# Kernel optimization log

Measured on AMD Instinct MI355X. Metric: run time of the kernel, lower is better.

## Reference

```python
import jax, jax.numpy as jnp
import numpy as np
import math

EMBED_DIM = 2048
NUM_HEADS = 32
GROUPS = 4
HEAD_DIM = EMBED_DIM // NUM_HEADS  # 64
HPG = NUM_HEADS // GROUPS          # heads per group = 8


def setup_inputs() -> dict:
    key = jax.random.key(0)
    k_x, k_wq, k_bq, k_wkv, k_bkv = jax.random.split(key, 5)
    B, L = 4, 4096
    scale = 1.0 / math.sqrt(EMBED_DIM)
    return {
        "x": jax.random.normal(k_x, (B, L, EMBED_DIM), dtype=jnp.float32),
        "Wq": jax.random.normal(k_wq, (EMBED_DIM, EMBED_DIM), dtype=jnp.float32) * scale,
        "bq": jax.random.normal(k_bq, (EMBED_DIM,), dtype=jnp.float32) * 0.01,
        "Wkv": jax.random.normal(k_wkv, (EMBED_DIM, 2 * HEAD_DIM * GROUPS), dtype=jnp.float32) * scale,
        "bkv": jax.random.normal(k_bkv, (2 * HEAD_DIM * GROUPS,), dtype=jnp.float32) * 0.01,
    }


def reference(x, Wq, bq, Wkv, bkv):
    B, L, _ = x.shape
    # projections
    q = (x @ Wq + bq).reshape(B, L, GROUPS, HPG, HEAD_DIM)          # blghd
    kv = (x @ Wkv + bkv).reshape(B, L, GROUPS, 2, HEAD_DIM)
    k, v = kv[:, :, :, 0], kv[:, :, :, 1]                            # blgd
    # scores: q @ k^T with k of shape (..., 1, head_dim) -> (..., HPG, 1)
    scores = jnp.einsum("blghd,blgd->blgh", q, k)[..., None] / math.sqrt(HEAD_DIM)
    attn = jax.nn.softmax(scores, axis=-1)                           # size-1 axis -> ones
    # attn @ v: (..., HPG, 1) @ (..., 1, head_dim) -> (..., HPG, head_dim)
    out = attn * v[:, :, :, None, :]                                 # blghd
    return out.reshape(B, L, EMBED_DIM)
```

## Files before the change

kernel.cpp:

```cpp
#include <hip/hip_runtime.h>


#define EMBED 2048
#define SV 272

typedef _Float16 half8 __attribute__((ext_vector_type(8)));
typedef _Float16 half4v __attribute__((ext_vector_type(4)));
typedef float f32x4 __attribute__((ext_vector_type(4)));

#define GLOAD16(g, l)                                                      \
  __builtin_amdgcn_global_load_lds(                                        \
      (const __attribute__((address_space(1))) void*)(g),                  \
      (__attribute__((address_space(3))) void*)(l), 16, 0, 0)

__global__ __launch_bounds__(256) void prep_b(const float* __restrict__ Wkv,
                                              _Float16* __restrict__ Bt) {
  const int t = threadIdx.x;
  const int kb = blockIdx.x * 4;
  const int vcol = ((t >> 6) * 128) + 64 + (t & 63);
  float v[4];
#pragma unroll
  for (int i = 0; i < 4; ++i) v[i] = Wkv[(size_t)(kb + i) * 512 + vcol];
  half4v h;
#pragma unroll
  for (int i = 0; i < 4; ++i) h[i] = (_Float16)v[i];
  *(half4v*)&Bt[(size_t)t * EMBED + kb] = h;
}

__global__ __launch_bounds__(256) void gqa_main(
    const float* __restrict__ x, const _Float16* __restrict__ Bt,
    const float* __restrict__ bkv, float* __restrict__ out) {
  __shared__ __align__(16) char smem[4 * 8192 + 4 * 16384];
  char* const Ab = smem;
  char* const Bb = smem + 4 * 8192;
  float* const Vs = (float*)smem;

  const int tid = threadIdx.x;
  const int w = tid >> 6;
  const int lane = tid & 63;
  const int lm = lane & 15;
  const int lq = lane >> 4;
  const int row0 = blockIdx.x * 64;

  const int acol = ((lane & 7) ^ (lane >> 3)) << 4;
  const char* asrc0 = (const char*)x +
      (size_t)(row0 + w * 16 + (lane >> 3)) * (EMBED * 4) + acol;
  const char* asrc1 = asrc0 + (size_t)8 * EMBED * 4;
  const int adst0 = (w * 16) * 128;
  const int bcol = (((lane & 3) << 4) ^ (((lane >> 3) & 3) << 4));
  const char* bsrc0 = (const char*)Bt +
      (size_t)(w * 64 + (lane >> 2)) * (EMBED * 2) + bcol;
  const int bdst0 = (w * 64) * 64;

#define STAGE(b, s)                                                        \
  {                                                                        \
    const size_t sa_ = (size_t)(s) * 128;          \
    GLOAD16(asrc0 + sa_, Ab + (b) * 8192 + adst0);                         \
    GLOAD16(asrc1 + sa_, Ab + (b) * 8192 + adst0 + 1024);                  \
    const size_t sb_ = (size_t)(s) * 64;           \
    GLOAD16(bsrc0 + sb_, Bb + (b) * 16384 + bdst0);                        \
    GLOAD16(bsrc0 + sb_ + (size_t)16 * EMBED * 2,                          \
            Bb + (b) * 16384 + bdst0 + 1024);                              \
    GLOAD16(bsrc0 + sb_ + (size_t)32 * EMBED * 2,                          \
            Bb + (b) * 16384 + bdst0 + 2048);                              \
    GLOAD16(bsrc0 + sb_ + (size_t)48 * EMBED * 2,                          \
            Bb + (b) * 16384 + bdst0 + 3072);                              \
  }

  const int arswz = (lm & 7) << 4;
  const int brswz = ((lm >> 1) & 3) << 4;

#define COMPUTE(b)                                                         \
  {                                                                        \
    const char* Ar_ = Ab + (b) * 8192 + lm * 128;                          \
    const char* Br_ = Bb + (b) * 16384 + (w * 64 + lm) * 64 +              \
                      ((lq << 4) ^ brswz);                                 \
    half8 bf_[4];                                                          \
    _Pragma("unroll") for (int ni = 0; ni < 4; ++ni)                       \
        bf_[ni] = *(const half8*)(Br_ + ni * 1024);                        \
    _Pragma("unroll") for (int mi = 0; mi < 4; ++mi) {                     \
      f32x4 a0_ = *(const f32x4*)(Ar_ + mi * 2048 + ((lq << 5) ^ arswz));  \
      f32x4 a1_ = *(const f32x4*)(Ar_ + mi * 2048 + (((lq << 5) + 16) ^ arswz)); \
      half8 af_;                                                           \
      _Pragma("unroll") for (int j = 0; j < 4; ++j) af_[j] = (_Float16)a0_[j]; \
      _Pragma("unroll") for (int j = 0; j < 4; ++j) af_[4 + j] = (_Float16)a1_[j]; \
      _Pragma("unroll") for (int ni = 0; ni < 4; ++ni)                     \
          acc[mi][ni] = __builtin_amdgcn_mfma_f32_16x16x32_f16(            \
              af_, bf_[ni], acc[mi][ni], 0, 0, 0);                         \
    }                                                                      \
  }

  f32x4 acc[4][4] = {};

  STAGE(0, 0);
  STAGE(1, 1);
  STAGE(2, 2);

  for (int tt = 0; tt < 64; tt += 4) {
#define ITER(T, BC, BS)                                                    \
    asm volatile("s_waitcnt vmcnt(12)" ::: "memory");                      \
    __builtin_amdgcn_s_barrier();                                          \
    {                                                                      \
      const int ss_ = (T) + 3 < 64 ? (T) + 3 : 63;                         \
      STAGE(BS, ss_);                                                      \
    }                                                                      \
    COMPUTE(BC);
    ITER(tt + 0, 0, 3)
    ITER(tt + 1, 1, 0)
    ITER(tt + 2, 2, 1)
    ITER(tt + 3, 3, 2)
#undef ITER
  }

  asm volatile("s_waitcnt vmcnt(0)" ::: "memory");
  __syncthreads();

  float bias[4];
#pragma unroll
  for (int ni = 0; ni < 4; ++ni) bias[ni] = bkv[w * 128 + 64 + ni * 16 + lm];

#pragma unroll
  for (int c = 0; c < 8; ++c) {
    const int mi = c >> 1;
    if ((lq >> 1) == (c & 1)) {
#pragma unroll
      for (int ni = 0; ni < 4; ++ni) {
        const int n = w * 64 + ni * 16 + lm;
        f32x4 v = acc[mi][ni];
#pragma unroll
        for (int r = 0; r < 4; ++r)
          Vs[((lq & 1) * 4 + r) * SV + n] = v[r] + bias[ni];
      }
    }
    __syncthreads();
    f32x4* out4 = (f32x4*)(out + (size_t)(row0 + c * 8) * EMBED);
#pragma unroll 4
    for (int i = 0; i < 16; ++i) {
      const int f = i * 256 + tid;
      const int row = f >> 9;
      const int c4 = f & 511;
      const int grp = c4 >> 7;
      const int d4 = c4 & 15;
      out4[(size_t)row * 512 + c4] =
          *(const f32x4*)&Vs[row * SV + grp * 64 + d4 * 4];
    }
    __syncthreads();
  }
}

extern "C" void kernel_launch(void* const* d_in, const int* in_sizes, int n_in,
                              void* d_out, int out_size, void* d_ws, size_t ws_size,
                              hipStream_t stream) {
  const float* x = (const float*)d_in[0];
  const float* Wkv = (const float*)d_in[3];
  const float* bkv = (const float*)d_in[4];
  float* out = (float*)d_out;
  _Float16* Bt = (_Float16*)d_ws;

  prep_b<<<512, 256, 0, stream>>>(Wkv, Bt);
  gqa_main<<<256, 256, 0, stream>>>(x, Bt, bkv, out);
}
```

Measured before the change: 265.9 us.

## Double K-depth per pipeline stage and split fragment loads from MFMA

Each pipeline stage now covers twice the K range, using 3 LDS buffers of 48KB instead of 4 buffers of 24KB, with prefetch distance reduced from 3 to 2. Each iteration loads the first half's fragments before issuing the next stage's global loads, then alternates MFMA with loading the second half. The aim is more bytes in flight per wave and fewer barriers per K, so the kernel hides global-memory latency better. The cost is a larger LDS footprint (144KB) and a shallower pipeline.

```diff
diff --git a/kernel.cpp b/kernel.cpp
--- a/kernel.cpp
+++ b/kernel.cpp
@@ -30,9 +30,9 @@
 __global__ __launch_bounds__(256) void gqa_main(
     const float* __restrict__ x, const _Float16* __restrict__ Bt,
     const float* __restrict__ bkv, float* __restrict__ out) {
-  __shared__ __align__(16) char smem[4 * 8192 + 4 * 16384];
+  __shared__ __align__(16) char smem[3 * 16384 + 3 * 32768];
   char* const Ab = smem;
-  char* const Bb = smem + 4 * 8192;
+  char* const Bb = smem + 3 * 16384;
   float* const Vs = (float*)smem;
 
   const int tid = threadIdx.x;
@@ -43,74 +43,91 @@
   const int row0 = blockIdx.x * 64;
 
   const int acol = ((lane & 7) ^ (lane >> 3)) << 4;
-  const char* asrc0 = (const char*)x +
+  const char* asrc = (const char*)x +
       (size_t)(row0 + w * 16 + (lane >> 3)) * (EMBED * 4) + acol;
-  const char* asrc1 = asrc0 + (size_t)8 * EMBED * 4;
   const int adst0 = (w * 16) * 128;
-  const int bcol = (((lane & 3) << 4) ^ (((lane >> 3) & 3) << 4));
-  const char* bsrc0 = (const char*)Bt +
+  const int bcol = (((lane & 3) ^ ((lane >> 3) & 3)) << 4);
+  const char* bsrc = (const char*)Bt +
       (size_t)(w * 64 + (lane >> 2)) * (EMBED * 2) + bcol;
   const int bdst0 = (w * 64) * 64;
 
 #define STAGE(b, s)                                                        \
   {                                                                        \
-    const size_t sa_ = (size_t)(s) * 128;          \
-    GLOAD16(asrc0 + sa_, Ab + (b) * 8192 + adst0);                         \
-    GLOAD16(asrc1 + sa_, Ab + (b) * 8192 + adst0 + 1024);                  \
-    const size_t sb_ = (size_t)(s) * 64;           \
-    GLOAD16(bsrc0 + sb_, Bb + (b) * 16384 + bdst0);                        \
-    GLOAD16(bsrc0 + sb_ + (size_t)16 * EMBED * 2,                          \
-            Bb + (b) * 16384 + bdst0 + 1024);                              \
-    GLOAD16(bsrc0 + sb_ + (size_t)32 * EMBED * 2,                          \
-            Bb + (b) * 16384 + bdst0 + 2048);                              \
-    GLOAD16(bsrc0 + sb_ + (size_t)48 * EMBED * 2,                          \
-            Bb + (b) * 16384 + bdst0 + 3072);                              \
+    const char* as_ = asrc + (size_t)(s) * 256;                            \
+    char* ad_ = Ab + (b) * 16384 + adst0;                                  \
+    GLOAD16(as_, ad_);                                                     \
+    GLOAD16(as_ + (size_t)8 * EMBED * 4, ad_ + 1024);                      \
+    GLOAD16(as_ + 128, ad_ + 8192);                                        \
+    GLOAD16(as_ + (size_t)8 * EMBED * 4 + 128, ad_ + 8192 + 1024);         \
+    const char* bs_ = bsrc + (size_t)(s) * 128;                            \
+    char* bd_ = Bb + (b) * 32768 + bdst0;                                  \
+    GLOAD16(bs_, bd_);                                                     \
+    GLOAD16(bs_ + (size_t)16 * EMBED * 2, bd_ + 1024);                     \
+    GLOAD16(bs_ + (size_t)32 * EMBED * 2, bd_ + 2048);                     \
+    GLOAD16(bs_ + (size_t)48 * EMBED * 2, bd_ + 3072);                     \
+    GLOAD16(bs_ + 64, bd_ + 16384);                                        \
+    GLOAD16(bs_ + (size_t)16 * EMBED * 2 + 64, bd_ + 16384 + 1024);        \
+    GLOAD16(bs_ + (size_t)32 * EMBED * 2 + 64, bd_ + 16384 + 2048);        \
+    GLOAD16(bs_ + (size_t)48 * EMBED * 2 + 64, bd_ + 16384 + 3072);        \
   }
 
   const int arswz = (lm & 7) << 4;
   const int brswz = ((lm >> 1) & 3) << 4;
 
-#define COMPUTE(b)                                                         \
+#define LOADFRAG(b, roa, rob)                                              \
   {                                                                        \
-    const char* Ar_ = Ab + (b) * 8192 + lm * 128;                          \
-    const char* Br_ = Bb + (b) * 16384 + (w * 64 + lm) * 64 +              \
+    const char* Ar_ = Ab + (b) * 16384 + (roa) + lm * 128;                 \
+    const char* Br_ = Bb + (b) * 32768 + (rob) + (w * 64 + lm) * 64 +      \
                       ((lq << 4) ^ brswz);                                 \
-    half8 bf_[4];                                                          \
     _Pragma("unroll") for (int ni = 0; ni < 4; ++ni)                       \
-        bf_[ni] = *(const half8*)(Br_ + ni * 1024);                        \
+        bfr_[ni] = *(const half8*)(Br_ + ni * 1024);                       \
     _Pragma("unroll") for (int mi = 0; mi < 4; ++mi) {                     \
-      f32x4 a0_ = *(const f32x4*)(Ar_ + mi * 2048 + ((lq << 5) ^ arswz));  \
-      f32x4 a1_ = *(const f32x4*)(Ar_ + mi * 2048 + (((lq << 5) + 16) ^ arswz)); \
-      half8 af_;                                                           \
-      _Pragma("unroll") for (int j = 0; j < 4; ++j) af_[j] = (_Float16)a0_[j]; \
-      _Pragma("unroll") for (int j = 0; j < 4; ++j) af_[4 + j] = (_Float16)a1_[j]; \
-      _Pragma("unroll") for (int ni = 0; ni < 4; ++ni)                     \
-          acc[mi][ni] = __builtin_amdgcn_mfma_f32_16x16x32_f16(            \
-              af_, bf_[ni], acc[mi][ni], 0, 0, 0);                         \
+      a0r_[mi] = *(const f32x4*)(Ar_ + mi * 2048 + ((lq << 5) ^ arswz));   \
+      a1r_[mi] =                                                           \
+          *(const f32x4*)(Ar_ + mi * 2048 + (((lq << 5) + 16) ^ arswz));   \
     }                                                                      \
+  }
+#define MFMAFRAG()                                                         \
+  _Pragma("unroll") for (int mi = 0; mi < 4; ++mi) {                       \
+    half8 af_;                                                             \
+    _Pragma("unroll") for (int j = 0; j < 4; ++j)                          \
+        af_[j] = (_Float16)a0r_[mi][j];                                    \
+    _Pragma("unroll") for (int j = 0; j < 4; ++j)                          \
+        af_[4 + j] = (_Float16)a1r_[mi][j];                                \
+    _Pragma("unroll") for (int ni = 0; ni < 4; ++ni)                       \
+        acc[mi][ni] = __builtin_amdgcn_mfma_f32_16x16x32_f16(              \
+            af_, bfr_[ni], acc[mi][ni], 0, 0, 0);                          \
   }
 
   f32x4 acc[4][4] = {};
 
   STAGE(0, 0);
   STAGE(1, 1);
-  STAGE(2, 2);
 
-  for (int tt = 0; tt < 64; tt += 4) {
 #define ITER(T, BC, BS)                                                    \
+  {                                                                        \
     asm volatile("s_waitcnt vmcnt(12)" ::: "memory");                      \
     __builtin_amdgcn_s_barrier();                                          \
+    f32x4 a0r_[4], a1r_[4];                                                \
+    half8 bfr_[4];                                                         \
+    LOADFRAG(BC, 0, 0);                                                    \
     {                                                                      \
-      const int ss_ = (T) + 3 < 64 ? (T) + 3 : 63;                         \
+      const int ss_ = (T) + 2 < 32 ? (T) + 2 : 31;                         \
       STAGE(BS, ss_);                                                      \
     }                                                                      \
-    COMPUTE(BC);
-    ITER(tt + 0, 0, 3)
+    MFMAFRAG();                                                            \
+    LOADFRAG(BC, 8192, 16384);                                             \
+    MFMAFRAG();                                                            \
+  }
+
+  for (int tt = 0; tt < 30; tt += 3) {
+    ITER(tt + 0, 0, 2)
     ITER(tt + 1, 1, 0)
     ITER(tt + 2, 2, 1)
-    ITER(tt + 3, 3, 2)
+  }
+  ITER(30, 0, 2)
+  ITER(31, 1, 0)
 #undef ITER
-  }
 
   asm volatile("s_waitcnt vmcnt(0)" ::: "memory");
   __syncthreads();
```

Measured after the change: 262.3 us. About the same (-1.3%).
